# Kernel tuning notes

Hardware: AMD Instinct MI355X
Metric: run time of the kernel (lower is better)

The kernel has to match this reference:

```python
import jax, jax.numpy as jnp
import numpy as np

B, C = 2, 4
SPATIAL = (128, 128, 128)
N_PTS = 32          # num_points_per_class
THR = 0.5           # threshold


def setup_inputs() -> dict:
    key = jax.random.key(0)
    logits = jax.random.normal(key, (B, C) + SPATIAL, dtype=jnp.float32)
    return {"logits": logits}


def _extract_points(logits):
    """Vectorized equivalent of the per-(batch,class) nonzero/topk loop.

    For every (b, c): softmax prob > THR defines candidates; top-k by prob
    selects up to N_PTS points. Classes are visited in the original order
    (foreground 1..C-1, then background 0); valid points are compacted to
    the front per batch element; padding has label -1 and coords 0.
    Output width is fixed at C*N_PTS (jit-friendly) instead of the batch
    max count, but all valid (coord, label) entries and their order match.
    """
    b, c = logits.shape[:2]
    spatial = logits.shape[2:]
    dims = len(spatial)
    S = int(np.prod(spatial))
    probs = jax.nn.softmax(logits, axis=1).reshape(b, c, S)  # [b,c,S]
    # class visitation order: 1..C-1 then 0 (background last)
    order = jnp.concatenate([jnp.arange(1, c), jnp.arange(1)])  # [c]
    probs = probs[:, order]                                    # [b,c,S]
    score = jnp.where(probs > THR, probs, -jnp.inf)
    top_vals, top_idx = jax.lax.top_k(score, N_PTS)            # [b,c,N_PTS]
    valid = top_vals > -jnp.inf                                # [b,c,N_PTS]
    coords = jnp.stack(jnp.unravel_index(top_idx, spatial), axis=-1)  # [b,c,N_PTS,dims]
    labels = jnp.where(valid, order[None, :, None], -1)        # [b,c,N_PTS]
    coords = jnp.where(valid[..., None], coords, 0)
    # flatten classes and compact valid points to the front (stable sort)
    N = c * N_PTS
    labels = labels.reshape(b, N)
    coords = coords.reshape(b, N, dims)
    perm = jnp.argsort((labels < 0).astype(jnp.int32), axis=1, stable=True)  # [b,N]
    labels = jnp.take_along_axis(labels, perm, axis=1)
    coords = jnp.take_along_axis(coords, perm[..., None], axis=1)
    return coords.astype(jnp.int32), labels.astype(jnp.int32)


def reference(logits):
    coords, labels = _extract_points(logits)
    return coords, labels
```

## Files before the change

### kernel.cpp

```cpp
#include <hip/hip_runtime.h>
#include <stdint.h>

#define Bn 2
#define Cn 4
#define Sn (128 * 128 * 128)
#define NPTS 32
#define NBINS 1025
#define THRf 0.5f
#define PB 4096
#define FCAP 2048

__device__ __forceinline__ int bin_of_bits(unsigned int u) {
    return (int)((u - 0x3F000000u) >> 13);
}

__device__ __forceinline__ void softmax_argmax4(float l0, float l1, float l2, float l3,
                                                int* cm_out, float* p_out) {
    float m = fmaxf(fmaxf(l0, l1), fmaxf(l2, l3));
    float e0 = expf(l0 - m);
    float e1 = expf(l1 - m);
    float e2 = expf(l2 - m);
    float e3 = expf(l3 - m);
    float s = ((e0 + e1) + e2) + e3;
    float em = e0; int cm = 0;
    if (e1 > em) { em = e1; cm = 1; }
    if (e2 > em) { em = e2; cm = 2; }
    if (e3 > em) { em = e3; cm = 3; }
    *cm_out = cm;
    *p_out = em / s;
}

__global__ __launch_bounds__(256) void fused_kernel(const float* __restrict__ logits,
                                                    unsigned int* __restrict__ cnt,
                                                    uint2* __restrict__ cand,
                                                    int cap) {
    __shared__ unsigned int lh[Cn * NBINS];
    __shared__ uint2 buf[PB];
    __shared__ unsigned int ccount;
    __shared__ unsigned int lcut[Cn];
    __shared__ unsigned int cls_cnt[Cn], cls_base[Cn], cls_pos[Cn];
    const int b = blockIdx.y;
    const int t = threadIdx.x;
    for (int j = t; j < Cn * NBINS; j += 256) lh[j] = 0u;
    if (t == 0) ccount = 0u;
    if (t < Cn) { lcut[t] = 0u; cls_cnt[t] = 0u; cls_pos[t] = 0u; }
    __syncthreads();

    const float* base = logits + (size_t)b * Cn * Sn;
    const float4* s0 = (const float4*)base;
    const float4* s1 = (const float4*)(base + Sn);
    const float4* s2 = (const float4*)(base + 2 * Sn);
    const float4* s3 = (const float4*)(base + 3 * Sn);
    const int qs = blockIdx.x * (PB / 4);
    #pragma unroll
    for (int it = 0; it < PB / 4 / 256; ++it) {
        int q = qs + it * 256 + t;
        float4 v0 = s0[q], v1 = s1[q], v2 = s2[q], v3 = s3[q];
        const float* a0 = &v0.x; const float* a1 = &v1.x;
        const float* a2 = &v2.x; const float* a3 = &v3.x;
        #pragma unroll
        for (int k = 0; k < 4; ++k) {
            int cm; float p;
            softmax_argmax4(a0[k], a1[k], a2[k], a3[k], &cm, &p);
            if (p > THRf) {
                unsigned int ub = __float_as_uint(p);
                atomicAdd(&lh[cm * NBINS + bin_of_bits(ub)], 1u);
                unsigned int pos = atomicAdd(&ccount, 1u);
                buf[pos] = make_uint2(ub, (unsigned int)(q * 4 + k) | ((unsigned int)cm << 21));
            }
        }
    }
    __syncthreads();

    {
        const int wave = t >> 6, lane = t & 63;
        const unsigned int* h = &lh[wave * NBINS];
        const int lo = lane * 17;
        unsigned int cs = 0;
        #pragma unroll
        for (int k = 0; k < 17; ++k) {
            int bin = lo + k;
            if (bin < NBINS) cs += h[bin];
        }
        unsigned int S = cs;
        #pragma unroll
        for (int off = 1; off < 64; off <<= 1) {
            unsigned int v = __shfl_down(S, off, 64);
            if (lane + off < 64) S += v;
        }
        unsigned int suf = S - cs;
        if (S >= NPTS && suf < NPTS) {
            unsigned int acc = suf;
            int hi = min(lo + 16, NBINS - 1);
            for (int bin = hi; bin >= lo; --bin) {
                acc += h[bin];
                if (acc >= NPTS) { lcut[wave] = (unsigned int)bin; break; }
            }
        }
    }
    __syncthreads();

    const unsigned int n = ccount;
    for (unsigned int j = t; j < n; j += 256) {
        uint2 e = buf[j];
        unsigned int cm = e.y >> 21;
        if ((unsigned int)bin_of_bits(e.x) >= lcut[cm])
            atomicAdd(&cls_cnt[cm], 1u);
    }
    __syncthreads();
    if (t < Cn && cls_cnt[t] > 0)
        cls_base[t] = atomicAdd(&cnt[b * Cn + t], cls_cnt[t]);
    __syncthreads();
    for (unsigned int j = t; j < n; j += 256) {
        uint2 e = buf[j];
        unsigned int cm = e.y >> 21;
        if ((unsigned int)bin_of_bits(e.x) >= lcut[cm]) {
            unsigned int pos = cls_base[cm] + atomicAdd(&cls_pos[cm], 1u);
            if (pos < (unsigned int)cap)
                cand[(size_t)(b * Cn + cm) * cap + pos] =
                    make_uint2(e.x, e.y & 0x1FFFFFu);
        }
    }
}

__global__ __launch_bounds__(1024) void select3(const unsigned int* __restrict__ cnt,
                                                const uint2* __restrict__ cand,
                                                int cap,
                                                unsigned int* __restrict__ validn,
                                                uint2* __restrict__ topk) {
    __shared__ unsigned int lh[NBINS];
    __shared__ uint2 fbuf[FCAP];
    __shared__ unsigned int s_m, s_T;
    const int bc = blockIdx.x, t = threadIdx.x;
    const int n = min((int)cnt[bc], cap);
    for (int j = t; j < NBINS; j += 1024) lh[j] = 0u;
    if (t == 0) { s_m = 0u; s_T = 0u; }
    __syncthreads();
    const uint2* src = cand + (size_t)bc * cap;
    for (int j = t; j < n; j += 1024)
        atomicAdd(&lh[bin_of_bits(src[j].x)], 1u);
    __syncthreads();
    if (t < 64) {
        const int lane = t;
        const int lo = lane * 17;
        unsigned int cs = 0;
        #pragma unroll
        for (int k = 0; k < 17; ++k) {
            int bin = lo + k;
            if (bin < NBINS) cs += lh[bin];
        }
        unsigned int S = cs;
        #pragma unroll
        for (int off = 1; off < 64; off <<= 1) {
            unsigned int v = __shfl_down(S, off, 64);
            if (lane + off < 64) S += v;
        }
        unsigned int suf = S - cs;
        if (S >= NPTS && suf < NPTS) {
            unsigned int acc = suf;
            int hi = min(lo + 16, NBINS - 1);
            for (int bin = hi; bin >= lo; --bin) {
                acc += lh[bin];
                if (acc >= NPTS) { s_T = (unsigned int)bin; break; }
            }
        }
    }
    __syncthreads();
    const unsigned int T = s_T;
    for (int j = t; j < n; j += 1024) {
        uint2 e = src[j];
        if ((unsigned int)bin_of_bits(e.x) >= T) {
            unsigned int pos = atomicAdd(&s_m, 1u);
            if (pos < FCAP) fbuf[pos] = e;
        }
    }
    __syncthreads();
    const int m = min((int)s_m, FCAP);
    const int vn = min(n, NPTS);
    if (t == 0) validn[bc] = (unsigned int)vn;
    for (int i = t; i < m; i += 1024) {
        uint2 e = fbuf[i];
        int rank = 0;
        for (int j = 0; j < m; ++j) {
            uint2 o = fbuf[j];
            rank += (int)((o.x > e.x) || (o.x == e.x && o.y < e.y));
        }
        if (rank < vn) topk[bc * NPTS + rank] = e;
    }
}

__global__ void emit_kernel(const uint2* __restrict__ topk,
                            const unsigned int* __restrict__ validn,
                            int* __restrict__ out) {
    const int b = blockIdx.x;
    __shared__ int pre[Cn + 1];
    if (threadIdx.x == 0) {
        int acc = 0;
        for (int oc = 0; oc < Cn; ++oc) {
            pre[oc] = acc;
            int c = (oc + 1) & 3;
            acc += (int)validn[b * Cn + c];
        }
        pre[Cn] = acc;
    }
    __syncthreads();
    const int j = threadIdx.x;
    int label = -1, z = 0, y = 0, x = 0;
    if (j < pre[Cn]) {
        int oc = 0;
        while (j >= pre[oc + 1]) ++oc;
        int c = (oc + 1) & 3;
        int r = j - pre[oc];
        uint2 e = topk[(b * Cn + c) * NPTS + r];
        int idx = (int)e.y;
        z = idx >> 14;
        y = (idx >> 7) & 127;
        x = idx & 127;
        label = c;
    }
    int* coords = out;
    int* labels = out + Bn * Cn * NPTS * 3;
    int base = b * Cn * NPTS + j;
    coords[base * 3 + 0] = z;
    coords[base * 3 + 1] = y;
    coords[base * 3 + 2] = x;
    labels[base] = label;
}

extern "C" void kernel_launch(void* const* d_in, const int* in_sizes, int n_in,
                              void* d_out, int out_size, void* d_ws, size_t ws_size,
                              hipStream_t stream) {
    const float* logits = (const float*)d_in[0];
    int* out = (int*)d_out;

    unsigned int* cnt = (unsigned int*)d_ws;
    unsigned int* validn = cnt + Bn * Cn;
    uint2* topk = (uint2*)(validn + Bn * Cn);
    uint2* cand = topk + Bn * Cn * NPTS;
    size_t fixed = (size_t)((char*)cand - (char*)d_ws);
    int cap = (int)((ws_size - fixed) / (Bn * Cn * sizeof(uint2)));
    if (cap > (1 << 18)) cap = 1 << 18;
    if (cap < 4096) cap = 4096;

    hipMemsetAsync(cnt, 0, Bn * Cn * sizeof(unsigned int), stream);

    dim3 grid(Sn / PB, Bn);
    fused_kernel<<<grid, 256, 0, stream>>>(logits, cnt, cand, cap);
    select3<<<Bn * Cn, 1024, 0, stream>>>(cnt, cand, cap, validn, topk);
    emit_kernel<<<Bn, 128, 0, stream>>>(topk, validn, out);
}
```

Baseline: 122.7 us.

## Aggregate LDS atomics per wave, widen blocks, fuse emit into select via last-block

The per-thread LDS atomics on the shared candidate counter and the per-class counters are replaced with wave-level ballot/popcount aggregation, so one lane does each atomic and the other lanes compute their offset with a prefix popcount. Block size goes from 256 to 512 threads, and the cutoff search is limited to the first four waves. The emit kernel is folded into the select kernel: a per-batch done counter picks the last finishing block, which writes the output. This drops one launch, at the cost of threadfence and an extra memset word.

```diff
diff --git a/kernel.cpp b/kernel.cpp
--- a/kernel.cpp
+++ b/kernel.cpp
@@ -8,6 +8,7 @@
 #define NBINS 1025
 #define THRf 0.5f
 #define PB 4096
+#define BT 512
 #define FCAP 2048
 
 __device__ __forceinline__ int bin_of_bits(unsigned int u) {
@@ -30,10 +31,10 @@
     *p_out = em / s;
 }
 
-__global__ __launch_bounds__(256) void fused_kernel(const float* __restrict__ logits,
-                                                    unsigned int* __restrict__ cnt,
-                                                    uint2* __restrict__ cand,
-                                                    int cap) {
+__global__ __launch_bounds__(BT) void fused_kernel(const float* __restrict__ logits,
+                                                   unsigned int* __restrict__ cnt,
+                                                   uint2* __restrict__ cand,
+                                                   int cap) {
     __shared__ unsigned int lh[Cn * NBINS];
     __shared__ uint2 buf[PB];
     __shared__ unsigned int ccount;
@@ -41,7 +42,8 @@
     __shared__ unsigned int cls_cnt[Cn], cls_base[Cn], cls_pos[Cn];
     const int b = blockIdx.y;
     const int t = threadIdx.x;
-    for (int j = t; j < Cn * NBINS; j += 256) lh[j] = 0u;
+    const int lane = t & 63;
+    for (int j = t; j < Cn * NBINS; j += BT) lh[j] = 0u;
     if (t == 0) ccount = 0u;
     if (t < Cn) { lcut[t] = 0u; cls_cnt[t] = 0u; cls_pos[t] = 0u; }
     __syncthreads();
@@ -53,8 +55,8 @@
     const float4* s3 = (const float4*)(base + 3 * Sn);
     const int qs = blockIdx.x * (PB / 4);
     #pragma unroll
-    for (int it = 0; it < PB / 4 / 256; ++it) {
-        int q = qs + it * 256 + t;
+    for (int it = 0; it < PB / 4 / BT; ++it) {
+        int q = qs + it * BT + t;
         float4 v0 = s0[q], v1 = s1[q], v2 = s2[q], v3 = s3[q];
         const float* a0 = &v0.x; const float* a1 = &v1.x;
         const float* a2 = &v2.x; const float* a3 = &v3.x;
@@ -62,76 +64,108 @@
         for (int k = 0; k < 4; ++k) {
             int cm; float p;
             softmax_argmax4(a0[k], a1[k], a2[k], a3[k], &cm, &p);
-            if (p > THRf) {
-                unsigned int ub = __float_as_uint(p);
-                atomicAdd(&lh[cm * NBINS + bin_of_bits(ub)], 1u);
-                unsigned int pos = atomicAdd(&ccount, 1u);
-                buf[pos] = make_uint2(ub, (unsigned int)(q * 4 + k) | ((unsigned int)cm << 21));
+            bool pass = p > THRf;
+            unsigned int ub = __float_as_uint(p);
+            if (pass) atomicAdd(&lh[cm * NBINS + bin_of_bits(ub)], 1u);
+            unsigned long long mk = __ballot(pass);
+            if (mk) {
+                unsigned int bs = 0;
+                if (lane == 0) bs = atomicAdd(&ccount, (unsigned int)__popcll(mk));
+                bs = __shfl(bs, 0, 64);
+                if (pass) {
+                    unsigned int pfx = (unsigned int)__popcll(mk & ((1ull << lane) - 1ull));
+                    buf[bs + pfx] = make_uint2(ub, (unsigned int)(q * 4 + k) |
+                                                   ((unsigned int)cm << 21));
+                }
             }
         }
     }
     __syncthreads();
 
     {
-        const int wave = t >> 6, lane = t & 63;
-        const unsigned int* h = &lh[wave * NBINS];
-        const int lo = lane * 17;
-        unsigned int cs = 0;
-        #pragma unroll
-        for (int k = 0; k < 17; ++k) {
-            int bin = lo + k;
-            if (bin < NBINS) cs += h[bin];
-        }
-        unsigned int S = cs;
-        #pragma unroll
-        for (int off = 1; off < 64; off <<= 1) {
-            unsigned int v = __shfl_down(S, off, 64);
-            if (lane + off < 64) S += v;
-        }
-        unsigned int suf = S - cs;
-        if (S >= NPTS && suf < NPTS) {
-            unsigned int acc = suf;
-            int hi = min(lo + 16, NBINS - 1);
-            for (int bin = hi; bin >= lo; --bin) {
-                acc += h[bin];
-                if (acc >= NPTS) { lcut[wave] = (unsigned int)bin; break; }
+        const int wave = t >> 6;
+        if (wave < Cn) {
+            const unsigned int* h = &lh[wave * NBINS];
+            const int lo = lane * 17;
+            unsigned int cs = 0;
+            #pragma unroll
+            for (int k = 0; k < 17; ++k) {
+                int bin = lo + k;
+                if (bin < NBINS) cs += h[bin];
+            }
+            unsigned int S = cs;
+            #pragma unroll
+            for (int off = 1; off < 64; off <<= 1) {
+                unsigned int v = __shfl_down(S, off, 64);
+                if (lane + off < 64) S += v;
+            }
+            unsigned int suf = S - cs;
+            if (S >= NPTS && suf < NPTS) {
+                unsigned int acc = suf;
+                int hi = min(lo + 16, NBINS - 1);
+                for (int bin = hi; bin >= lo; --bin) {
+                    acc += h[bin];
+                    if (acc >= NPTS) { lcut[wave] = (unsigned int)bin; break; }
+                }
             }
         }
     }
     __syncthreads();
 
     const unsigned int n = ccount;
-    for (unsigned int j = t; j < n; j += 256) {
-        uint2 e = buf[j];
+    for (unsigned int j0 = 0; j0 < n; j0 += BT) {
+        unsigned int j = j0 + t;
+        bool v = j < n;
+        uint2 e = v ? buf[j] : make_uint2(0u, 0u);
         unsigned int cm = e.y >> 21;
-        if ((unsigned int)bin_of_bits(e.x) >= lcut[cm])
-            atomicAdd(&cls_cnt[cm], 1u);
+        bool pass = v && ((unsigned int)bin_of_bits(e.x) >= lcut[cm]);
+        #pragma unroll
+        for (int c = 0; c < Cn; ++c) {
+            unsigned long long mk = __ballot(pass && cm == (unsigned int)c);
+            if (mk && lane == 0) atomicAdd(&cls_cnt[c], (unsigned int)__popcll(mk));
+        }
     }
     __syncthreads();
     if (t < Cn && cls_cnt[t] > 0)
         cls_base[t] = atomicAdd(&cnt[b * Cn + t], cls_cnt[t]);
     __syncthreads();
-    for (unsigned int j = t; j < n; j += 256) {
-        uint2 e = buf[j];
+    for (unsigned int j0 = 0; j0 < n; j0 += BT) {
+        unsigned int j = j0 + t;
+        bool v = j < n;
+        uint2 e = v ? buf[j] : make_uint2(0u, 0u);
         unsigned int cm = e.y >> 21;
-        if ((unsigned int)bin_of_bits(e.x) >= lcut[cm]) {
-            unsigned int pos = cls_base[cm] + atomicAdd(&cls_pos[cm], 1u);
-            if (pos < (unsigned int)cap)
-                cand[(size_t)(b * Cn + cm) * cap + pos] =
-                    make_uint2(e.x, e.y & 0x1FFFFFu);
-        }
-    }
-}
-
-__global__ __launch_bounds__(1024) void select3(const unsigned int* __restrict__ cnt,
-                                                const uint2* __restrict__ cand,
-                                                int cap,
-                                                unsigned int* __restrict__ validn,
-                                                uint2* __restrict__ topk) {
+        bool pass = v && ((unsigned int)bin_of_bits(e.x) >= lcut[cm]);
+        #pragma unroll
+        for (int c = 0; c < Cn; ++c) {
+            unsigned long long mk = __ballot(pass && cm == (unsigned int)c);
+            if (mk) {
+                unsigned int wb = 0;
+                if (lane == 0) wb = atomicAdd(&cls_pos[c], (unsigned int)__popcll(mk));
+                wb = __shfl(wb, 0, 64);
+                if (pass && cm == (unsigned int)c) {
+                    unsigned int pfx = (unsigned int)__popcll(mk & ((1ull << lane) - 1ull));
+                    unsigned int pos = cls_base[c] + wb + pfx;
+                    if (pos < (unsigned int)cap)
+                        cand[(size_t)(b * Cn + c) * cap + pos] =
+                            make_uint2(e.x, e.y & 0x1FFFFFu);
+                }
+            }
+        }
+    }
+}
+
+__global__ __launch_bounds__(1024) void select_emit(const unsigned int* __restrict__ cnt,
+                                                    const uint2* __restrict__ cand,
+                                                    int cap,
+                                                    unsigned int* __restrict__ validn,
+                                                    uint2* __restrict__ topk,
+                                                    unsigned int* __restrict__ done,
+                                                    int* __restrict__ out) {
     __shared__ unsigned int lh[NBINS];
     __shared__ uint2 fbuf[FCAP];
-    __shared__ unsigned int s_m, s_T;
+    __shared__ unsigned int s_m, s_T, s_old;
     const int bc = blockIdx.x, t = threadIdx.x;
+    const int b = bc >> 2;
     const int n = min((int)cnt[bc], cap);
     for (int j = t; j < NBINS; j += 1024) lh[j] = 0u;
     if (t == 0) { s_m = 0u; s_T = 0u; }
@@ -187,44 +221,47 @@
         }
         if (rank < vn) topk[bc * NPTS + rank] = e;
     }
-}
-
-__global__ void emit_kernel(const uint2* __restrict__ topk,
-                            const unsigned int* __restrict__ validn,
-                            int* __restrict__ out) {
-    const int b = blockIdx.x;
-    __shared__ int pre[Cn + 1];
-    if (threadIdx.x == 0) {
-        int acc = 0;
-        for (int oc = 0; oc < Cn; ++oc) {
-            pre[oc] = acc;
-            int c = (oc + 1) & 3;
-            acc += (int)validn[b * Cn + c];
-        }
-        pre[Cn] = acc;
-    }
-    __syncthreads();
-    const int j = threadIdx.x;
-    int label = -1, z = 0, y = 0, x = 0;
-    if (j < pre[Cn]) {
-        int oc = 0;
-        while (j >= pre[oc + 1]) ++oc;
-        int c = (oc + 1) & 3;
-        int r = j - pre[oc];
-        uint2 e = topk[(b * Cn + c) * NPTS + r];
-        int idx = (int)e.y;
-        z = idx >> 14;
-        y = (idx >> 7) & 127;
-        x = idx & 127;
-        label = c;
-    }
-    int* coords = out;
-    int* labels = out + Bn * Cn * NPTS * 3;
-    int base = b * Cn * NPTS + j;
-    coords[base * 3 + 0] = z;
-    coords[base * 3 + 1] = y;
-    coords[base * 3 + 2] = x;
-    labels[base] = label;
+
+    __threadfence();
+    __syncthreads();
+    if (t == 0) s_old = atomicAdd(&done[b], 1u);
+    __syncthreads();
+    if (s_old == 3u) {
+        __threadfence();
+        __shared__ int pre[Cn + 1];
+        if (t == 0) {
+            int acc = 0;
+            for (int oc = 0; oc < Cn; ++oc) {
+                pre[oc] = acc;
+                acc += (int)validn[b * Cn + ((oc + 1) & 3)];
+            }
+            pre[Cn] = acc;
+        }
+        __syncthreads();
+        if (t < Cn * NPTS) {
+            const int j = t;
+            int label = -1, z = 0, y = 0, x = 0;
+            if (j < pre[Cn]) {
+                int oc = 0;
+                while (j >= pre[oc + 1]) ++oc;
+                int c = (oc + 1) & 3;
+                int r = j - pre[oc];
+                uint2 e = topk[(b * Cn + c) * NPTS + r];
+                int idx = (int)e.y;
+                z = idx >> 14;
+                y = (idx >> 7) & 127;
+                x = idx & 127;
+                label = c;
+            }
+            int* coords = out;
+            int* labels = out + Bn * Cn * NPTS * 3;
+            int bo = b * Cn * NPTS + j;
+            coords[bo * 3 + 0] = z;
+            coords[bo * 3 + 1] = y;
+            coords[bo * 3 + 2] = x;
+            labels[bo] = label;
+        }
+    }
 }
 
 extern "C" void kernel_launch(void* const* d_in, const int* in_sizes, int n_in,
@@ -234,7 +271,8 @@
     int* out = (int*)d_out;
 
     unsigned int* cnt = (unsigned int*)d_ws;
-    unsigned int* validn = cnt + Bn * Cn;
+    unsigned int* done = cnt + Bn * Cn;
+    unsigned int* validn = done + Bn;
     uint2* topk = (uint2*)(validn + Bn * Cn);
     uint2* cand = topk + Bn * Cn * NPTS;
     size_t fixed = (size_t)((char*)cand - (char*)d_ws);
@@ -242,10 +280,9 @@
     if (cap > (1 << 18)) cap = 1 << 18;
     if (cap < 4096) cap = 4096;
 
-    hipMemsetAsync(cnt, 0, Bn * Cn * sizeof(unsigned int), stream);
+    hipMemsetAsync(cnt, 0, (Bn * Cn + Bn) * sizeof(unsigned int), stream);
 
     dim3 grid(Sn / PB, Bn);
-    fused_kernel<<<grid, 256, 0, stream>>>(logits, cnt, cand, cap);
-    select3<<<Bn * Cn, 1024, 0, stream>>>(cnt, cand, cap, validn, topk);
-    emit_kernel<<<Bn, 128, 0, stream>>>(topk, validn, out);
-}
+    fused_kernel<<<grid, BT, 0, stream>>>(logits, cnt, cand, cap);
+    select_emit<<<Bn * Cn, 1024, 0, stream>>>(cnt, cand, cap, validn, topk, done, out);
+}
```

After: 130.6 us. +6.4%, slower.
